# Kernel optimization log

Measured on AMD Instinct MI355X. Metric: run time of the kernel, lower is better.

## Reference

```python
import jax, jax.numpy as jnp
import numpy as np

B, L, C, K = 8, 16384, 512, 31


def setup_inputs() -> dict:
    key = jax.random.key(0)
    k1, k2 = jax.random.split(key)
    x = jax.random.normal(k1, (B, L, C), dtype=jnp.float32)
    # Matches tf kernel shape (K, dim, 1); Glorot-ish scale.
    kernel = jax.random.normal(k2, (K, C, 1), dtype=jnp.float32) * (1.0 / np.sqrt(K * C))
    bias = jnp.zeros((C,), dtype=jnp.float32)
    return {"x": x, "kernel": kernel, "bias": bias}


def reference(x, kernel, bias):
    # Original loops over channels doing per-channel conv1d; that is exactly a
    # depthwise conv1d (channel multiplier 1), expressed here as one grouped conv.
    c = x.shape[-1]
    rhs = jnp.transpose(kernel, (0, 2, 1))  # [K, C, 1] -> [K, 1, C] (W, I/group, O)
    out = jax.lax.conv_general_dilated(
        x, rhs,
        window_strides=(1,),
        padding="SAME",
        dimension_numbers=("NWC", "WIO", "NWC"),
        feature_group_count=c,
    )
    return out + bias[None, None, :]
```

## Files before the change

kernel.cpp:

```cpp
#include <hip/hip_runtime.h>


#define BB 8
#define LL 16384
#define CC 512
#define KK 31
#define PAD 15
#define TL 16
#define TILES_PER_B (LL / TL)

__global__ __launch_bounds__(256)
void depthconv1d_2680059592713_kernel(const float* __restrict__ x,
                                      const float* __restrict__ w,
                                      const float* __restrict__ bias,
                                      float* __restrict__ out) {
    const int c2   = threadIdx.x;
    const int tile = blockIdx.x;
    const int b    = tile >> 10;
    const int l0   = (tile & (TILES_PER_B - 1)) * TL;
    const int c    = c2 * 2;

    float2 wk[KK];
#pragma unroll
    for (int k = 0; k < KK; ++k) {
        wk[k] = *(const float2*)(w + k * CC + c);
    }

    const float2 bv = *(const float2*)(bias + c);

    float2 acc[TL];
#pragma unroll
    for (int t = 0; t < TL; ++t) acc[t] = bv;

    const float* xb = x + ((size_t)b * LL) * CC + c;

#pragma unroll
    for (int i = 0; i < TL + KK - 1; ++i) {
        const int li = l0 + i - PAD;
        float2 xv;
        if (li >= 0 && li < LL) {
            xv = *(const float2*)(xb + (size_t)li * CC);
        } else {
            xv = make_float2(0.f, 0.f);
        }
#pragma unroll
        for (int t = 0; t < TL; ++t) {
            const int k = i - t;
            if (k >= 0 && k < KK) {
                acc[t].x = fmaf(xv.x, wk[k].x, acc[t].x);
                acc[t].y = fmaf(xv.y, wk[k].y, acc[t].y);
            }
        }
    }

    float* ob = out + (((size_t)b * LL) + l0) * CC + c;
#pragma unroll
    for (int t = 0; t < TL; ++t) {
        *(float2*)(ob + (size_t)t * CC) = acc[t];
    }
}

extern "C" void kernel_launch(void* const* d_in, const int* in_sizes, int n_in,
                              void* d_out, int out_size, void* d_ws, size_t ws_size,
                              hipStream_t stream) {
    const float* x    = (const float*)d_in[0];
    const float* w    = (const float*)d_in[1];
    const float* bias = (const float*)d_in[2];
    float* out        = (float*)d_out;

    const int n_blocks = BB * TILES_PER_B;
    hipLaunchKernelGGL(depthconv1d_2680059592713_kernel,
                       dim3(n_blocks), dim3(256), 0, stream,
                       x, w, bias, out);
}
```

Measured before the change: 461.6 us.

## Stream rows through a register ring buffer with larger tiles and XCD-aware block mapping

New measurement: 454.4 us. No clear change (-1.6%).

```diff
diff --git a/kernel.cpp b/kernel.cpp
--- a/kernel.cpp
+++ b/kernel.cpp
@@ -6,57 +6,72 @@
 #define CC 512
 #define KK 31
 #define PAD 15
-#define TL 16
+#define TL 64
 #define TILES_PER_B (LL / TL)
+#define NWG (BB * TILES_PER_B)
+#define PD 4
+#define WIN 32
 
 __global__ __launch_bounds__(256)
 void depthconv1d_2680059592713_kernel(const float* __restrict__ x,
                                       const float* __restrict__ w,
                                       const float* __restrict__ bias,
                                       float* __restrict__ out) {
-    const int c2   = threadIdx.x;
-    const int tile = blockIdx.x;
-    const int b    = tile >> 10;
+    const int c2 = threadIdx.x;
+    const int d  = blockIdx.x;
+    const int tile = (d & 7) * (NWG / 8) + (d >> 3);
+    const int b    = tile >> 8;
     const int l0   = (tile & (TILES_PER_B - 1)) * TL;
     const int c    = c2 * 2;
+
+    const float* xb = x + ((size_t)b * LL) * CC + c;
+
+    auto loadrow = [&](int r) -> float2 {
+        const int lr = l0 + r;
+        if (lr >= 0 && lr < LL) {
+            return *(const float2*)(xb + (size_t)lr * CC);
+        }
+        return make_float2(0.f, 0.f);
+    };
+
+    float2 xw[WIN];
+#pragma unroll
+    for (int r = -PAD; r <= PAD; ++r) {
+        xw[r & (WIN - 1)] = loadrow(r);
+    }
+
+    float2 tmp[PD];
+#pragma unroll
+    for (int p = 0; p < PD; ++p) {
+        tmp[p] = loadrow(PAD + 1 + p);
+    }
 
     float2 wk[KK];
 #pragma unroll
     for (int k = 0; k < KK; ++k) {
         wk[k] = *(const float2*)(w + k * CC + c);
     }
-
     const float2 bv = *(const float2*)(bias + c);
 
-    float2 acc[TL];
+    float* ob = out + (((size_t)b * LL) + l0) * CC + c;
+
+#pragma unroll 1
+    for (int base = 0; base < TL; base += WIN) {
 #pragma unroll
-    for (int t = 0; t < TL; ++t) acc[t] = bv;
+        for (int j = 0; j < WIN; ++j) {
+            xw[(j + PAD + 1) & (WIN - 1)] = tmp[j & (PD - 1)];
+            tmp[j & (PD - 1)] = loadrow(base + j + PAD + 1 + PD);
 
-    const float* xb = x + ((size_t)b * LL) * CC + c;
+            float2 acc = bv;
+#pragma unroll
+            for (int k = 0; k < KK; ++k) {
+                const float2 xv = xw[(j + k - PAD) & (WIN - 1)];
+                acc.x = fmaf(xv.x, wk[k].x, acc.x);
+                acc.y = fmaf(xv.y, wk[k].y, acc.y);
+            }
 
-#pragma unroll
-    for (int i = 0; i < TL + KK - 1; ++i) {
-        const int li = l0 + i - PAD;
-        float2 xv;
-        if (li >= 0 && li < LL) {
-            xv = *(const float2*)(xb + (size_t)li * CC);
-        } else {
-            xv = make_float2(0.f, 0.f);
+            *(float2*)(ob + (size_t)(base + j) * CC) = acc;
         }
-#pragma unroll
-        for (int t = 0; t < TL; ++t) {
-            const int k = i - t;
-            if (k >= 0 && k < KK) {
-                acc[t].x = fmaf(xv.x, wk[k].x, acc[t].x);
-                acc[t].y = fmaf(xv.y, wk[k].y, acc[t].y);
-            }
-        }
-    }
-
-    float* ob = out + (((size_t)b * LL) + l0) * CC + c;
-#pragma unroll
-    for (int t = 0; t < TL; ++t) {
-        *(float2*)(ob + (size_t)t * CC) = acc[t];
     }
 }
 
@@ -68,8 +83,7 @@
     const float* bias = (const float*)d_in[2];
     float* out        = (float*)d_out;
 
-    const int n_blocks = BB * TILES_PER_B;
     hipLaunchKernelGGL(depthconv1d_2680059592713_kernel,
-                       dim3(n_blocks), dim3(256), 0, stream,
+                       dim3(NWG), dim3(256), 0, stream,
                        x, w, bias, out);
 }
```
